# Kernel tuning notes

Measured on AMD Instinct MI355X. Metric: run time of the kernel, lower is better.

The kernel has to match this reference:

```python
import jax, jax.numpy as jnp
import numpy as np

ROPE_THETA = 10000.0
N_KV_HEADS = 8


def _rope(x, pos, theta):
    # x: [..., D] with interleaved (even, odd) rotation pairs; pos: scalar position
    D = x.shape[-1]
    freqs = theta ** (-jnp.arange(0, D, 2, dtype=jnp.float32) / D)  # [D/2]
    ang = pos * freqs
    cos, sin = jnp.cos(ang), jnp.sin(ang)
    x1, x2 = x[..., 0::2], x[..., 1::2]
    return jnp.stack([x1 * cos - x2 * sin, x1 * sin + x2 * cos], axis=-1).reshape(x.shape)


def setup_inputs() -> dict:
    key = jax.random.key(0)
    ks = jax.random.split(key, 5)
    B, DIM, CACHE_LEN, HD = 32, 4096, 4096, 128
    N_HEADS = 32
    qkv_out = (N_HEADS + 2 * N_KV_HEADS) * HD  # 6144
    return {
        "x": jax.random.normal(ks[0], (B, DIM), dtype=jnp.float32),
        "cache_k": jax.random.normal(ks[1], (B, CACHE_LEN, N_KV_HEADS, HD), dtype=jnp.float32),
        "cache_v": jax.random.normal(ks[2], (B, CACHE_LEN, N_KV_HEADS, HD), dtype=jnp.float32),
        "wqkv": jax.random.normal(ks[3], (qkv_out, DIM), dtype=jnp.float32) * 0.02,
        "wo": jax.random.normal(ks[4], (DIM, DIM), dtype=jnp.float32) * 0.02,
        "ctx_len": 4095,
    }


def reference(x, cache_k, cache_v, wqkv, wo, ctx_len):
    B = x.shape[0]
    n_kv = cache_k.shape[2]
    hd = cache_k.shape[3]
    n_heads = (wqkv.shape[0] - 2 * n_kv * hd) // hd
    hpg = n_heads // n_kv  # heads per kv group

    # fused QKV projection
    xqkv = x @ wqkv.T  # [B, (n_heads + 2*n_kv)*hd]
    nq = n_heads * hd
    nk = n_kv * hd
    q = xqkv[:, :nq].reshape(B, n_kv, hpg, hd)
    k = xqkv[:, nq:nq + nk].reshape(B, n_kv, hd)
    v = xqkv[:, nq + nk:].reshape(B, n_kv, hd)

    # rope fused with KV-cache write: new token at position ctx_len
    q = _rope(q, ctx_len, ROPE_THETA)
    k = _rope(k, ctx_len, ROPE_THETA)
    cache_k = cache_k.at[:, ctx_len].set(k)
    cache_v = cache_v.at[:, ctx_len].set(v)

    T = ctx_len + 1  # valid cache length (python int -> static slice)
    K = cache_k[:, :T]  # [B, T, n_kv, hd]
    V = cache_v[:, :T]

    # GQA attention: q [b, g, h, d], K/V [b, t, g, d]
    scores = jnp.einsum("bghd,btgd->bght", q, K) / jnp.sqrt(jnp.float32(hd))
    w = jax.nn.softmax(scores, axis=-1)
    o = jnp.einsum("bght,btgd->bghd", w, V).reshape(B, n_heads * hd)
    return o @ wo.T
```

## Files before the change

kernel.cpp:

```cpp
#include <hip/hip_runtime.h>
#include <math.h>

#define BATCH 32
#define DIM   4096
#define CLEN  4096
#define HD    128
#define NKV   8
#define NHEAD 32
#define QKVN  6144
#define KVSTR (NKV * HD)
#define GN    64
#define KSEG  128
#define KSTG  4
#define KTOT  512
#define NSEG  8
#define NCH   16
#define TC    256
#define NSLOT 16
#define MNEG  -1.0e30f
#define SMASK -3.0e38f

template <int CTRL>
__device__ __forceinline__ float dpp_add(float x) {
  int y = __builtin_amdgcn_update_dpp(0, __float_as_int(x), CTRL, 0xF, 0xF, true);
  return x + __int_as_float(y);
}

__device__ __forceinline__ float half_reduce(float s) {
  s = dpp_add<0xB1>(s);
  s = dpp_add<0x4E>(s);
  s = dpp_add<0x124>(s);
  s = dpp_add<0x128>(s);
  s += __int_as_float(__builtin_amdgcn_ds_swizzle(__float_as_int(s), 0x401F));
  return s;
}

__device__ __forceinline__ float xhalf32(float v, int lane) {
  return __int_as_float(__builtin_amdgcn_ds_bpermute((lane ^ 32) << 2, __float_as_int(v)));
}

__global__ __launch_bounds__(256)
void gemm_partial(const float* __restrict__ X, const float* __restrict__ W,
                  float* __restrict__ part, const int N) {
  __shared__ float xs[KSEG * 32];
  __shared__ float wl[KSEG * 64];
  const int tid = threadIdx.x;
  const int c   = tid & 31;
  const int r   = tid >> 5;
  const int cx7 = c & 7;
  const int n0  = blockIdx.x * GN;
  const int k00 = blockIdx.y * KTOT;
  const int bq8 = tid & 7;
  const int tq  = tid >> 3;
  const int nqq = tq >> 1;
  const int nqo = (tq & 1) << 1;

  float a00=0,a01=0, a10=0,a11=0, a20=0,a21=0, a30=0,a31=0;

  float* xwp  = xs + (c * 4) * 32 + ((r ^ cx7) << 2);
  float* wwp0 = wl + (c * 4) * 64 + ((r ^ cx7) << 2);
  float* wwp1 = wwp0 + 32;

  for (int kk = 0; kk < KSTG; ++kk) {
    const int k0 = k00 + kk * KSEG;
    const float* Xp = X + (size_t)(r * 4) * DIM + k0 + c * 4;
    const float4 xv0 = *(const float4*)(Xp);
    const float4 xv1 = *(const float4*)(Xp + DIM);
    const float4 xv2 = *(const float4*)(Xp + 2 * DIM);
    const float4 xv3 = *(const float4*)(Xp + 3 * DIM);
    const float* Wp0 = W + (size_t)(n0 + r * 4) * DIM + k0 + c * 4;
    const float4 wv00 = *(const float4*)(Wp0);
    const float4 wv01 = *(const float4*)(Wp0 + DIM);
    const float4 wv02 = *(const float4*)(Wp0 + 2 * DIM);
    const float4 wv03 = *(const float4*)(Wp0 + 3 * DIM);
    const float* Wp1 = Wp0 + (size_t)32 * DIM;
    const float4 wv10 = *(const float4*)(Wp1);
    const float4 wv11 = *(const float4*)(Wp1 + DIM);
    const float4 wv12 = *(const float4*)(Wp1 + 2 * DIM);
    const float4 wv13 = *(const float4*)(Wp1 + 3 * DIM);

    if (kk) __syncthreads();

    *(float4*)(xwp + 0)   = make_float4(xv0.x, xv1.x, xv2.x, xv3.x);
    *(float4*)(xwp + 32)  = make_float4(xv0.y, xv1.y, xv2.y, xv3.y);
    *(float4*)(xwp + 64)  = make_float4(xv0.z, xv1.z, xv2.z, xv3.z);
    *(float4*)(xwp + 96)  = make_float4(xv0.w, xv1.w, xv2.w, xv3.w);
    *(float4*)(wwp0 + 0)   = make_float4(wv00.x, wv01.x, wv02.x, wv03.x);
    *(float4*)(wwp0 + 64)  = make_float4(wv00.y, wv01.y, wv02.y, wv03.y);
    *(float4*)(wwp0 + 128) = make_float4(wv00.z, wv01.z, wv02.z, wv03.z);
    *(float4*)(wwp0 + 192) = make_float4(wv00.w, wv01.w, wv02.w, wv03.w);
    *(float4*)(wwp1 + 0)   = make_float4(wv10.x, wv11.x, wv12.x, wv13.x);
    *(float4*)(wwp1 + 64)  = make_float4(wv10.y, wv11.y, wv12.y, wv13.y);
    *(float4*)(wwp1 + 128) = make_float4(wv10.z, wv11.z, wv12.z, wv13.z);
    *(float4*)(wwp1 + 192) = make_float4(wv10.w, wv11.w, wv12.w, wv13.w);
    __syncthreads();

#pragma unroll 8
    for (int k2 = 0; k2 < KSEG / 4; ++k2) {
      const int g = k2 & 7;
      const float* xr = xs + (k2 * 4) * 32 + ((bq8 ^ g) << 2);
      const float* wr = wl + (k2 * 4) * 64 + ((nqq ^ g) << 2) + nqo;
#pragma unroll
      for (int j = 0; j < 4; ++j) {
        const float4 xv = *(const float4*)(xr + j * 32);
        const float2 wv = *(const float2*)(wr + j * 64);
        a00 = fmaf(xv.x, wv.x, a00); a01 = fmaf(xv.x, wv.y, a01);
        a10 = fmaf(xv.y, wv.x, a10); a11 = fmaf(xv.y, wv.y, a11);
        a20 = fmaf(xv.z, wv.x, a20); a21 = fmaf(xv.z, wv.y, a21);
        a30 = fmaf(xv.w, wv.x, a30); a31 = fmaf(xv.w, wv.y, a31);
      }
    }
  }
  const int bq = bq8 << 2;
  const int nq = tq << 1;
  float* base = part + ((size_t)blockIdx.y * BATCH + bq) * N + n0 + nq;
  *(float2*)(base)         = make_float2(a00, a01);
  *(float2*)(base + N)     = make_float2(a10, a11);
  *(float2*)(base + 2 * N) = make_float2(a20, a21);
  *(float2*)(base + 3 * N) = make_float2(a30, a31);
}

__global__ __launch_bounds__(256)
void qkv_combine(const float* __restrict__ part, const int* __restrict__ ctxp,
                 float* __restrict__ qw, float* __restrict__ kn, float* __restrict__ vn) {
  const int idx = blockIdx.x * 256 + threadIdx.x;
  const int b  = idx / (QKVN / 2);
  const int c  = idx % (QKVN / 2);
  const int n0 = c * 2;
  float v0 = 0.f, v1 = 0.f;
#pragma unroll
  for (int s = 0; s < NSEG; ++s) {
    const float2 pv = *(const float2*)(part + ((size_t)s * BATCH + b) * QKVN + n0);
    v0 += pv.x; v1 += pv.y;
  }
  const float pos = (float)ctxp[0];
  const float L2T_OVER_64 = 0.20762050593045952f;
  if (n0 < DIM) {
    const int i = (n0 & 127) >> 1;
    const float fr = exp2f(-(float)i * L2T_OVER_64);
    float sn, cs; sincosf(pos * fr, &sn, &cs);
    qw[(size_t)b * DIM + n0]     = v0 * cs - v1 * sn;
    qw[(size_t)b * DIM + n0 + 1] = v0 * sn + v1 * cs;
  } else if (n0 < DIM + NKV * HD) {
    const int nk = n0 - DIM;
    const int i = (nk & 127) >> 1;
    const float fr = exp2f(-(float)i * L2T_OVER_64);
    float sn, cs; sincosf(pos * fr, &sn, &cs);
    kn[(size_t)b * (NKV * HD) + nk]     = v0 * cs - v1 * sn;
    kn[(size_t)b * (NKV * HD) + nk + 1] = v0 * sn + v1 * cs;
  } else {
    const int nv = n0 - DIM - NKV * HD;
    vn[(size_t)b * (NKV * HD) + nv]     = v0;
    vn[(size_t)b * (NKV * HD) + nv + 1] = v1;
  }
}

__device__ __forceinline__ void load8(float4 kb[4], float4 vb[4],
    const float* __restrict__ ckb, const float* __restrict__ cvb,
    const float* __restrict__ knr, const float* __restrict__ vnr,
    const int t0, const int half, const int ctx, const bool edge) {
#pragma unroll
  for (int u = 0; u < 4; ++u) {
    const int tr = t0 + u * 2 + half;
    const float* kp = ckb + (size_t)tr * KVSTR;
    const float* vp = cvb + (size_t)tr * KVSTR;
    if (edge) {
      if (tr == ctx) { kp = knr; vp = vnr; }
    }
    kb[u] = *(const float4*)kp;
    vb[u] = *(const float4*)vp;
  }
}

__device__ __forceinline__ void compute8(const float4 kb[4], const float4 vb[4],
    const float4 q[4], const int t0, const int half, const int ctx, const bool edge,
    float m[4], float l[4], float4 acc[4]) {
#pragma unroll
  for (int u = 0; u < 4; ++u) {
    float s[4];
#pragma unroll
    for (int hh = 0; hh < 4; ++hh) {
      float d = fmaf(kb[u].x, q[hh].x, kb[u].y * q[hh].y);
      d = fmaf(kb[u].z, q[hh].z, d);
      d = fmaf(kb[u].w, q[hh].w, d);
      s[hh] = half_reduce(d);
    }
    if (edge) {
      const int tr = t0 + u * 2 + half;
      if (tr > ctx) { s[0] = SMASK; s[1] = SMASK; s[2] = SMASK; s[3] = SMASK; }
    }
    if ((s[0] > m[0]) | (s[1] > m[1]) | (s[2] > m[2]) | (s[3] > m[3])) {
#pragma unroll
      for (int hh = 0; hh < 4; ++hh) {
        const float mn = fmaxf(m[hh], s[hh]);
        const float rs = __expf(m[hh] - mn);
        l[hh] *= rs;
        acc[hh].x *= rs; acc[hh].y *= rs; acc[hh].z *= rs; acc[hh].w *= rs;
        m[hh] = mn;
      }
    }
#pragma unroll
    for (int hh = 0; hh < 4; ++hh) {
      const float p = __expf(s[hh] - m[hh]);
      l[hh] += p;
      acc[hh].x = fmaf(p, vb[u].x, acc[hh].x);
      acc[hh].y = fmaf(p, vb[u].y, acc[hh].y);
      acc[hh].z = fmaf(p, vb[u].z, acc[hh].z);
      acc[hh].w = fmaf(p, vb[u].w, acc[hh].w);
    }
  }
}

__global__ __launch_bounds__(256)
void attn_fd(const float* __restrict__ qw, const float* __restrict__ knew,
             const float* __restrict__ vnew, const float* __restrict__ ck,
             const float* __restrict__ cv, const int* __restrict__ ctxp,
             float* __restrict__ opart, float* __restrict__ mlp) {
  const int bg   = blockIdx.x;
  const int b = bg >> 3, g = bg & 7;
  const int wid  = threadIdx.x >> 6;
  const int lane = threadIdx.x & 63;
  const int half = lane >> 5;
  const int d4   = (lane & 31) << 2;
  const int cidx = blockIdx.y * 4 + wid;
  const int ctx  = ctxp[0];
  const int c0   = cidx * TC;

  const float sc = 0.08838834764831845f;
  float4 q[4];
#pragma unroll
  for (int hh = 0; hh < 4; ++hh) {
    q[hh] = *(const float4*)(qw + ((size_t)b * NHEAD + g * 4 + hh) * HD + d4);
    q[hh].x *= sc; q[hh].y *= sc; q[hh].z *= sc; q[hh].w *= sc;
  }
  const float* ckb = ck + ((size_t)b * CLEN * NKV + g) * HD + d4;
  const float* cvb = cv + ((size_t)b * CLEN * NKV + g) * HD + d4;
  const float* knr = knew + ((size_t)b * NKV + g) * HD + d4;
  const float* vnr = vnew + ((size_t)b * NKV + g) * HD + d4;

  float m[4] = {MNEG, MNEG, MNEG, MNEG};
  float l[4] = {0.f, 0.f, 0.f, 0.f};
  float4 acc[4] = {};

  float4 kA[4], vA[4], kB[4], vB[4];
  int t = c0;
  load8(kA, vA, ckb, cvb, knr, vnr, t, half, ctx, t + 8 > ctx);
  for (int it = 0; it < TC / 16; ++it) {
    const int tb = t + 8;
    load8(kB, vB, ckb, cvb, knr, vnr, tb, half, ctx, tb + 8 > ctx);
    compute8(kA, vA, q, t, half, ctx, t + 8 > ctx, m, l, acc);
    const int tn = t + 16;
    if (it + 1 < TC / 16)
      load8(kA, vA, ckb, cvb, knr, vnr, tn, half, ctx, tn + 8 > ctx);
    compute8(kB, vB, q, tb, half, ctx, tb + 8 > ctx, m, l, acc);
    t = tn;
  }

#pragma unroll
  for (int hh = 0; hh < 4; ++hh) {
    const float mo = xhalf32(m[hh], lane);
    const float lo = xhalf32(l[hh], lane);
    float4 ao;
    ao.x = xhalf32(acc[hh].x, lane); ao.y = xhalf32(acc[hh].y, lane);
    ao.z = xhalf32(acc[hh].z, lane); ao.w = xhalf32(acc[hh].w, lane);
    const float mc = fmaxf(m[hh], mo);
    const float wa = __expf(m[hh] - mc);
    const float wb = __expf(mo - mc);
    l[hh] = wa * l[hh] + wb * lo;
    acc[hh].x = wa * acc[hh].x + wb * ao.x;
    acc[hh].y = wa * acc[hh].y + wb * ao.y;
    acc[hh].z = wa * acc[hh].z + wb * ao.z;
    acc[hh].w = wa * acc[hh].w + wb * ao.w;
    m[hh] = mc;
  }
  if (half == 0) {
#pragma unroll
    for (int hh = 0; hh < 4; ++hh) {
      const int hid = b * NHEAD + g * 4 + hh;
      const size_t slot = (size_t)hid * NSLOT + cidx;
      *(float4*)(opart + slot * HD + d4) = acc[hh];
      if ((lane & 31) == 0) { mlp[slot * 2] = m[hh]; mlp[slot * 2 + 1] = l[hh]; }
    }
  }
}

__global__ __launch_bounds__(128)
void attn_combine(const float* __restrict__ opart, const float* __restrict__ mlp,
                  float* __restrict__ ow) {
  const int p = blockIdx.x;
  const int d = threadIdx.x;
  float M = MNEG;
#pragma unroll
  for (int c = 0; c < NSLOT; ++c) M = fmaxf(M, mlp[((size_t)p * NSLOT + c) * 2]);
  float L = 0.f, O = 0.f;
#pragma unroll 8
  for (int c = 0; c < NSLOT; ++c) {
    const float mi = mlp[((size_t)p * NSLOT + c) * 2];
    const float w = __expf(mi - M);
    L += w * mlp[((size_t)p * NSLOT + c) * 2 + 1];
    O += w * opart[((size_t)p * NSLOT + c) * HD + d];
  }
  ow[(size_t)p * HD + d] = O / L;
}

__global__ __launch_bounds__(256)
void sum_partials(const float* __restrict__ part, float* __restrict__ out,
                  const int total4, const int nseg, const int stride) {
  const int i = blockIdx.x * 256 + threadIdx.x;
  if (i >= total4) return;
  float4 s = make_float4(0.f, 0.f, 0.f, 0.f);
  for (int g = 0; g < nseg; ++g) {
    const float4 v = *(const float4*)(part + (size_t)g * stride + (size_t)i * 4);
    s.x += v.x; s.y += v.y; s.z += v.z; s.w += v.w;
  }
  *(float4*)(out + (size_t)i * 4) = s;
}

extern "C" void kernel_launch(void* const* d_in, const int* in_sizes, int n_in,
                              void* d_out, int out_size, void* d_ws, size_t ws_size,
                              hipStream_t stream) {
  const float* x    = (const float*)d_in[0];
  const float* ck   = (const float*)d_in[1];
  const float* cv   = (const float*)d_in[2];
  const float* wqkv = (const float*)d_in[3];
  const float* wo   = (const float*)d_in[4];
  const int*   ctx  = (const int*)d_in[5];

  float* ws    = (float*)d_ws;
  float* pqkv  = ws;
  float* qw    = pqkv + (size_t)NSEG * BATCH * QKVN;
  float* kn    = qw + (size_t)BATCH * DIM;
  float* vn    = kn + (size_t)BATCH * NKV * HD;
  float* opart = vn + (size_t)BATCH * NKV * HD;
  float* mlp   = opart + (size_t)1024 * NSLOT * HD;
  float* ow    = mlp + (size_t)1024 * NSLOT * 2;
  float* pout  = pqkv;

  gemm_partial<<<dim3(QKVN / GN, NSEG), 256, 0, stream>>>(x, wqkv, pqkv, QKVN);
  qkv_combine<<<dim3(BATCH * QKVN / 2 / 256), 256, 0, stream>>>(pqkv, ctx, qw, kn, vn);
  attn_fd<<<dim3(BATCH * NKV, NCH / 4), 256, 0, stream>>>(qw, kn, vn, ck, cv, ctx, opart, mlp);
  attn_combine<<<dim3(BATCH * NHEAD), HD, 0, stream>>>(opart, mlp, ow);
  gemm_partial<<<dim3(DIM / GN, NSEG), 256, 0, stream>>>(ow, wo, pout, DIM);
  sum_partials<<<dim3((BATCH * DIM / 4 + 255) / 256), 256, 0, stream>>>(
      pout, (float*)d_out, BATCH * DIM / 4, NSEG, BATCH * DIM);
}
```

Before: 278.4 us.

## Widen GEMM N-tile to 128 with 4x4 register tiles and row-major swizzled W

The split-K GEMM now gives each block 128 output columns instead of 64 and halves the K range per block, which doubles the number of K segments. W is stored row-major in LDS with an XOR swizzle, and each thread computes a 4x4 output tile using float4 reads of both operands, so each LDS load feeds more FMAs. The cost is more partial-sum traffic, because 16 segments are written and then reduced in the combine kernel, plus higher register pressure from 16 in-flight W float4 loads and 16 accumulators.

New measurement: 332.1 us. +19.3%, slower.

```diff
diff --git a/kernel.cpp b/kernel.cpp
--- a/kernel.cpp
+++ b/kernel.cpp
@@ -9,11 +9,11 @@
 #define NHEAD 32
 #define QKVN  6144
 #define KVSTR (NKV * HD)
-#define GN    64
+#define GN    128
 #define KSEG  128
-#define KSTG  4
-#define KTOT  512
-#define NSEG  8
+#define KSTG  2
+#define KTOT  256
+#define NSEG  16
 #define NCH   16
 #define TC    256
 #define NSLOT 16
@@ -43,23 +43,19 @@
 void gemm_partial(const float* __restrict__ X, const float* __restrict__ W,
                   float* __restrict__ part, const int N) {
   __shared__ float xs[KSEG * 32];
-  __shared__ float wl[KSEG * 64];
+  __shared__ float wl[GN * KSEG];
   const int tid = threadIdx.x;
   const int c   = tid & 31;
   const int r   = tid >> 5;
   const int cx7 = c & 7;
   const int n0  = blockIdx.x * GN;
   const int k00 = blockIdx.y * KTOT;
-  const int bq8 = tid & 7;
-  const int tq  = tid >> 3;
-  const int nqq = tq >> 1;
-  const int nqo = (tq & 1) << 1;
-
-  float a00=0,a01=0, a10=0,a11=0, a20=0,a21=0, a30=0,a31=0;
-
-  float* xwp  = xs + (c * 4) * 32 + ((r ^ cx7) << 2);
-  float* wwp0 = wl + (c * 4) * 64 + ((r ^ cx7) << 2);
-  float* wwp1 = wwp0 + 32;
+  const int bq  = tid & 7;
+  const int nr  = tid >> 3;
+  const int rq  = nr & 7;
+
+  float acc[4][4] = {};
+  float* xwp = xs + (c * 4) * 32 + ((r ^ cx7) << 2);
 
   for (int kk = 0; kk < KSTG; ++kk) {
     const int k0 = k00 + kk * KSEG;
@@ -68,56 +64,67 @@
     const float4 xv1 = *(const float4*)(Xp + DIM);
     const float4 xv2 = *(const float4*)(Xp + 2 * DIM);
     const float4 xv3 = *(const float4*)(Xp + 3 * DIM);
-    const float* Wp0 = W + (size_t)(n0 + r * 4) * DIM + k0 + c * 4;
-    const float4 wv00 = *(const float4*)(Wp0);
-    const float4 wv01 = *(const float4*)(Wp0 + DIM);
-    const float4 wv02 = *(const float4*)(Wp0 + 2 * DIM);
-    const float4 wv03 = *(const float4*)(Wp0 + 3 * DIM);
-    const float* Wp1 = Wp0 + (size_t)32 * DIM;
-    const float4 wv10 = *(const float4*)(Wp1);
-    const float4 wv11 = *(const float4*)(Wp1 + DIM);
-    const float4 wv12 = *(const float4*)(Wp1 + 2 * DIM);
-    const float4 wv13 = *(const float4*)(Wp1 + 3 * DIM);
+    float4 wg[16];
+#pragma unroll
+    for (int it = 0; it < 16; ++it) {
+      const int q = tid + it * 256;
+      const int row = q >> 5, cc = q & 31;
+      wg[it] = *(const float4*)(W + (size_t)(n0 + row) * DIM + k0 + cc * 4);
+    }
 
     if (kk) __syncthreads();
 
-    *(float4*)(xwp + 0)   = make_float4(xv0.x, xv1.x, xv2.x, xv3.x);
-    *(float4*)(xwp + 32)  = make_float4(xv0.y, xv1.y, xv2.y, xv3.y);
-    *(float4*)(xwp + 64)  = make_float4(xv0.z, xv1.z, xv2.z, xv3.z);
-    *(float4*)(xwp + 96)  = make_float4(xv0.w, xv1.w, xv2.w, xv3.w);
-    *(float4*)(wwp0 + 0)   = make_float4(wv00.x, wv01.x, wv02.x, wv03.x);
-    *(float4*)(wwp0 + 64)  = make_float4(wv00.y, wv01.y, wv02.y, wv03.y);
-    *(float4*)(wwp0 + 128) = make_float4(wv00.z, wv01.z, wv02.z, wv03.z);
-    *(float4*)(wwp0 + 192) = make_float4(wv00.w, wv01.w, wv02.w, wv03.w);
-    *(float4*)(wwp1 + 0)   = make_float4(wv10.x, wv11.x, wv12.x, wv13.x);
-    *(float4*)(wwp1 + 64)  = make_float4(wv10.y, wv11.y, wv12.y, wv13.y);
-    *(float4*)(wwp1 + 128) = make_float4(wv10.z, wv11.z, wv12.z, wv13.z);
-    *(float4*)(wwp1 + 192) = make_float4(wv10.w, wv11.w, wv12.w, wv13.w);
+    *(float4*)(xwp + 0)  = make_float4(xv0.x, xv1.x, xv2.x, xv3.x);
+    *(float4*)(xwp + 32) = make_float4(xv0.y, xv1.y, xv2.y, xv3.y);
+    *(float4*)(xwp + 64) = make_float4(xv0.z, xv1.z, xv2.z, xv3.z);
+    *(float4*)(xwp + 96) = make_float4(xv0.w, xv1.w, xv2.w, xv3.w);
+#pragma unroll
+    for (int it = 0; it < 16; ++it) {
+      const int q = tid + it * 256;
+      const int row = q >> 5, cc = q & 31;
+      *(float4*)&wl[row * KSEG + ((cc ^ ((row >> 2) & 7)) << 2)] = wg[it];
+    }
     __syncthreads();
 
 #pragma unroll 8
-    for (int k2 = 0; k2 < KSEG / 4; ++k2) {
-      const int g = k2 & 7;
-      const float* xr = xs + (k2 * 4) * 32 + ((bq8 ^ g) << 2);
-      const float* wr = wl + (k2 * 4) * 64 + ((nqq ^ g) << 2) + nqo;
+    for (int k2 = 0; k2 < 32; ++k2) {
+      const float* xr = xs + (k2 * 4) * 32 + ((bq ^ (k2 & 7)) << 2);
+      float4 xv[4];
+#pragma unroll
+      for (int i = 0; i < 4; ++i) xv[i] = *(const float4*)(xr + i * 32);
+      const int wq = (k2 ^ rq) << 2;
+      float4 wv[4];
+#pragma unroll
+      for (int j = 0; j < 4; ++j)
+        wv[j] = *(const float4*)&wl[(nr * 4 + j) * KSEG + wq];
 #pragma unroll
       for (int j = 0; j < 4; ++j) {
-        const float4 xv = *(const float4*)(xr + j * 32);
-        const float2 wv = *(const float2*)(wr + j * 64);
-        a00 = fmaf(xv.x, wv.x, a00); a01 = fmaf(xv.x, wv.y, a01);
-        a10 = fmaf(xv.y, wv.x, a10); a11 = fmaf(xv.y, wv.y, a11);
-        a20 = fmaf(xv.z, wv.x, a20); a21 = fmaf(xv.z, wv.y, a21);
-        a30 = fmaf(xv.w, wv.x, a30); a31 = fmaf(xv.w, wv.y, a31);
+        const float4 w4 = wv[j];
+        acc[0][j] = fmaf(xv[0].x, w4.x, acc[0][j]);
+        acc[1][j] = fmaf(xv[0].y, w4.x, acc[1][j]);
+        acc[2][j] = fmaf(xv[0].z, w4.x, acc[2][j]);
+        acc[3][j] = fmaf(xv[0].w, w4.x, acc[3][j]);
+        acc[0][j] = fmaf(xv[1].x, w4.y, acc[0][j]);
+        acc[1][j] = fmaf(xv[1].y, w4.y, acc[1][j]);
+        acc[2][j] = fmaf(xv[1].z, w4.y, acc[2][j]);
+        acc[3][j] = fmaf(xv[1].w, w4.y, acc[3][j]);
+        acc[0][j] = fmaf(xv[2].x, w4.z, acc[0][j]);
+        acc[1][j] = fmaf(xv[2].y, w4.z, acc[1][j]);
+        acc[2][j] = fmaf(xv[2].z, w4.z, acc[2][j]);
+        acc[3][j] = fmaf(xv[2].w, w4.z, acc[3][j]);
+        acc[0][j] = fmaf(xv[3].x, w4.w, acc[0][j]);
+        acc[1][j] = fmaf(xv[3].y, w4.w, acc[1][j]);
+        acc[2][j] = fmaf(xv[3].z, w4.w, acc[2][j]);
+        acc[3][j] = fmaf(xv[3].w, w4.w, acc[3][j]);
       }
     }
   }
-  const int bq = bq8 << 2;
-  const int nq = tq << 1;
-  float* base = part + ((size_t)blockIdx.y * BATCH + bq) * N + n0 + nq;
-  *(float2*)(base)         = make_float2(a00, a01);
-  *(float2*)(base + N)     = make_float2(a10, a11);
-  *(float2*)(base + 2 * N) = make_float2(a20, a21);
-  *(float2*)(base + 3 * N) = make_float2(a30, a31);
+
+#pragma unroll
+  for (int bi = 0; bi < 4; ++bi) {
+    *(float4*)(part + ((size_t)blockIdx.y * BATCH + bq * 4 + bi) * N + n0 + nr * 4) =
+        make_float4(acc[bi][0], acc[bi][1], acc[bi][2], acc[bi][3]);
+  }
 }
 
 __global__ __launch_bounds__(256)
@@ -128,7 +135,7 @@
   const int c  = idx % (QKVN / 2);
   const int n0 = c * 2;
   float v0 = 0.f, v1 = 0.f;
-#pragma unroll
+#pragma unroll 8
   for (int s = 0; s < NSEG; ++s) {
     const float2 pv = *(const float2*)(part + ((size_t)s * BATCH + b) * QKVN + n0);
     v0 += pv.x; v1 += pv.y;
```
